# Optimization experiments

Measured on AMD Instinct MI355X. Metric: run time of the kernel, lower is better.

The kernel has to match this reference:

```python
import jax, jax.numpy as jnp
import numpy as np

BS, SEQ, DK = 4, 4096, 128

def setup_inputs() -> dict:
    key = jax.random.key(0)
    kq, kk, kv = jax.random.split(key, 3)
    q = jax.random.normal(kq, (BS, SEQ, DK), dtype=jnp.float32)
    k = jax.random.normal(kk, (BS, SEQ, DK), dtype=jnp.float32)
    v = jax.random.normal(kv, (BS, SEQ, DK), dtype=jnp.float32)
    return {"q": q, "k": k, "v": v}

def reference(q, k, v):
    d_k = q.shape[-1]
    # scores: [bs, s_q, s_k]
    scaled = jnp.einsum('bqd,bkd->bqk', q, k) / jnp.sqrt(jnp.asarray(d_k, q.dtype))
    # NOTE: original torch code applies softmax over dim=1 (query axis), faithfully reproduced here.
    attn = jax.nn.softmax(scaled, axis=1)
    return jnp.einsum('bqk,bkd->bqd', attn, v)
```

## Files before the change

### kernel.cpp

```cpp
#include <hip/hip_runtime.h>
#include <hip/hip_bf16.h>

#define BS  4
#define SEQ 4096
#define DK  128

#define C1_SCALE (1.4426950408889634f / 11.313708498984761f)

typedef __attribute__((ext_vector_type(8))) short bf16x8;
typedef __attribute__((ext_vector_type(4))) float f32x4;
typedef unsigned short ushort_t;

__device__ inline unsigned pk_bf16(float a, float b) {
    __hip_bfloat162 h = __float22bfloat162_rn(make_float2(a, b));
    union { __hip_bfloat162 h2; unsigned u; } cv;
    cv.h2 = h;
    return cv.u;
}

__device__ inline bf16x8 pk8(float4 a, float4 b) {
    union { bf16x8 v; unsigned u[4]; } r;
    r.u[0] = pk_bf16(a.x, a.y);
    r.u[1] = pk_bf16(a.z, a.w);
    r.u[2] = pk_bf16(b.x, b.y);
    r.u[3] = pk_bf16(b.z, b.w);
    return r.v;
}

__global__ __launch_bounds__(256) void cast_qk_sw(
    const float* __restrict__ Q, const float* __restrict__ K,
    ushort_t* __restrict__ Qb, ushort_t* __restrict__ Kb)
{
    const int g = blockIdx.x * 256 + threadIdx.x;
    const int q = g >> 4, ap = g & 15;
    const int a = ap ^ (q & 15);
    const float* src = Q + (size_t)q * DK + a * 8;
    float4 x = *(const float4*)src, y = *(const float4*)(src + 4);
    *(bf16x8*)(Qb + (size_t)g * 8) = pk8(x, y);
    src = K + (size_t)q * DK + a * 8;
    x = *(const float4*)src; y = *(const float4*)(src + 4);
    *(bf16x8*)(Kb + (size_t)g * 8) = pk8(x, y);
}

__global__ __launch_bounds__(256) void sdpa_lsum(
    const ushort_t* __restrict__ Qb, const ushort_t* __restrict__ Kb,
    float* __restrict__ lp)
{
    const int kt = blockIdx.x, qs = blockIdx.y, b = blockIdx.z;
    const int tid = threadIdx.x;
    const int w = tid >> 6, lane = tid & 63, ln = lane & 15, quad = lane >> 4;

    bf16x8 ka[2][4];
#pragma unroll
    for (int mt = 0; mt < 2; ++mt)
#pragma unroll
        for (int c = 0; c < 4; ++c)
            ka[mt][c] = *(const bf16x8*)(Kb +
                ((size_t)(b * SEQ) + kt * 128 + w * 32 + mt * 16 + ln) * DK +
                (((c * 4 + quad) ^ ln) * 8));

    float ls[2][4] = {};
    const ushort_t* qbase = Qb + ((size_t)(b * SEQ) + qs * 512 + ln) * DK;
    bf16x8 qf0[2][4], qf1[2][4];

#define L_PRE(QF, IT)                                                          \
    {                                                                          \
        _Pragma("unroll")                                                      \
        for (int nt = 0; nt < 2; ++nt)                                         \
            _Pragma("unroll")                                                  \
            for (int c = 0; c < 4; ++c)                                        \
                QF[nt][c] = *(const bf16x8*)(qbase +                           \
                    ((size_t)((IT) * 32 + nt * 16)) * DK +                     \
                    (((c * 4 + quad) ^ ln) * 8));                              \
    }
#define L_CMP(QF)                                                              \
    {                                                                          \
        _Pragma("unroll")                                                      \
        for (int mt = 0; mt < 2; ++mt)                                         \
            _Pragma("unroll")                                                  \
            for (int nt = 0; nt < 2; ++nt) {                                   \
                f32x4 s = {0.f, 0.f, 0.f, 0.f};                                \
                _Pragma("unroll")                                              \
                for (int c = 0; c < 4; ++c)                                    \
                    s = __builtin_amdgcn_mfma_f32_16x16x32_bf16(               \
                        ka[mt][c], QF[nt][c], s, 0, 0, 0);                     \
                _Pragma("unroll")                                              \
                for (int r = 0; r < 4; ++r)                                    \
                    ls[mt][r] += __builtin_amdgcn_exp2f(C1_SCALE * s[r]);      \
            }                                                                  \
    }
    L_PRE(qf0, 0)
    for (int ii = 0; ii < 8; ++ii) {
        const int i0 = 2 * ii;
        L_PRE(qf1, i0 + 1)
        L_CMP(qf0)
        if (ii < 7) L_PRE(qf0, i0 + 2)
        L_CMP(qf1)
    }
#undef L_PRE
#undef L_CMP

#pragma unroll
    for (int mt = 0; mt < 2; ++mt)
#pragma unroll
        for (int r = 0; r < 4; ++r) {
            float vv = ls[mt][r];
            vv += __shfl_xor(vv, 1);
            vv += __shfl_xor(vv, 2);
            vv += __shfl_xor(vv, 4);
            vv += __shfl_xor(vv, 8);
            ls[mt][r] = vv;
        }
    if (ln < 8) {
        int k = kt * 128 + w * 32 + (ln >> 2) * 16 + quad * 4 + (ln & 3);
        lp[((size_t)(qs * BS + b)) * SEQ + k] = ls[ln >> 2][ln & 3];
    }
}

__global__ __launch_bounds__(256) void vb_transpose(
    const float* __restrict__ V, const float* __restrict__ lp,
    ushort_t* __restrict__ VbT)
{
    __shared__ float Vl[64][132];
    __shared__ float Wl[64];

    const int kt = blockIdx.x, b = blockIdx.y;
    const int tid = threadIdx.x;
    const int k0 = kt * 64;
    {
        int r = tid >> 2, sg = tid & 3;
        const float* src = V + ((size_t)(b * SEQ) + k0 + r) * DK + sg * 32;
#pragma unroll
        for (int i = 0; i < 8; ++i)
            *(float4*)&Vl[r][sg * 32 + i * 4] = *(const float4*)(src + i * 4);
    }
    if (tid < 64) {
        float s = 0.f;
#pragma unroll
        for (int qs = 0; qs < 8; ++qs)
            s += lp[((size_t)(qs * BS + b)) * SEQ + k0 + tid];
        Wl[tid] = 1.0f / s;
    }
    __syncthreads();

    const int d = tid >> 1, kh = tid & 1;
    unsigned u[16];
#pragma unroll
    for (int j = 0; j < 16; ++j) {
        int row = kh * 32 + j * 2;
        u[j] = pk_bf16(Vl[row][d] * Wl[row], Vl[row + 1][d] * Wl[row + 1]);
    }
    ushort_t* dst = VbT + ((size_t)(b * DK) + d) * SEQ + k0 + kh * 32;
#pragma unroll
    for (int i = 0; i < 4; ++i) {
        uint4 t4; t4.x = u[i*4]; t4.y = u[i*4+1]; t4.z = u[i*4+2]; t4.w = u[i*4+3];
        *(uint4*)(dst + i * 8) = t4;
    }
}

__global__ __launch_bounds__(256) void sdpa_out(
    const ushort_t* __restrict__ Qb, const ushort_t* __restrict__ Kb,
    const ushort_t* __restrict__ VbT,
    float* __restrict__ Op, float* __restrict__ O, int use_partial)
{
    __shared__ ushort_t Pt[2][64 * 64];

    const int g  = blockIdx.x;
    const int qt = blockIdx.y;
    const int ks = g >> 2, b = g & 3;
    const int tid = threadIdx.x;
    const int w = tid >> 6, lane = tid & 63, ln = lane & 15, quad = lane >> 4;

    bf16x8 qa[4][4];
#pragma unroll
    for (int nt = 0; nt < 4; ++nt)
#pragma unroll
        for (int c = 0; c < 4; ++c)
            qa[c][nt] = *(const bf16x8*)(Qb +
                ((size_t)(b * SEQ) + qt * 64 + nt * 16 + ln) * DK +
                (((c * 4 + quad) ^ ln) * 8));

    f32x4 acc[4][2];
#pragma unroll
    for (int i = 0; i < 4; ++i)
#pragma unroll
        for (int j = 0; j < 2; ++j) acc[i][j] = (f32x4){0.f, 0.f, 0.f, 0.f};

    const ushort_t* kfp = Kb + ((size_t)(b * SEQ) + ks * 1024 + w * 16 + ln) * DK;
    const ushort_t* vfp = VbT + ((size_t)(b * DK) + w * 32 + ln) * SEQ + ks * 1024 + quad * 8;

    bf16x8 kf0[4], kf1[4], vf0[4], vf1[4];

#define QK_PHASE(P, KF)                                                        \
    {                                                                          \
        _Pragma("unroll")                                                      \
        for (int nt = 0; nt < 4; ++nt) {                                       \
            f32x4 s = {0.f, 0.f, 0.f, 0.f};                                    \
            _Pragma("unroll")                                                  \
            for (int c = 0; c < 4; ++c)                                        \
                s = __builtin_amdgcn_mfma_f32_16x16x32_bf16(KF[c], qa[c][nt], s, 0, 0, 0); \
            uint2 pw;                                                          \
            pw.x = pk_bf16(__builtin_amdgcn_exp2f(C1_SCALE * s[0]),            \
                           __builtin_amdgcn_exp2f(C1_SCALE * s[1]));           \
            pw.y = pk_bf16(__builtin_amdgcn_exp2f(C1_SCALE * s[2]),            \
                           __builtin_amdgcn_exp2f(C1_SCALE * s[3]));           \
            const int q = nt * 16 + ln;                                        \
            const int a16 = w * 2 + (quad >> 1);                               \
            *(uint2*)&Pt[P][q * 64 + ((a16 ^ (q & 7)) * 8) + (quad & 1) * 4] = pw; \
        }                                                                      \
    }
#define PREFETCH(KF, VF, I1)                                                   \
    {                                                                          \
        _Pragma("unroll")                                                      \
        for (int c = 0; c < 4; ++c)                                            \
            KF[c] = *(const bf16x8*)(kfp + (size_t)(I1) * 64 * DK +            \
                                     (((c * 4 + quad) ^ ln) * 8));             \
        _Pragma("unroll")                                                      \
        for (int dt = 0; dt < 2; ++dt)                                         \
            _Pragma("unroll")                                                  \
            for (int kc = 0; kc < 2; ++kc)                                     \
                VF[kc * 2 + dt] = *(const bf16x8*)(vfp +                       \
                    (size_t)dt * 16 * SEQ + (size_t)(I1) * 64 + kc * 32);      \
    }
#define PV_PHASE(P, VF)                                                        \
    {                                                                          \
        _Pragma("unroll")                                                      \
        for (int kc = 0; kc < 2; ++kc) {                                       \
            bf16x8 pa[4];                                                      \
            _Pragma("unroll")                                                  \
            for (int qf2 = 0; qf2 < 4; ++qf2)                                  \
                pa[qf2] = *(const bf16x8*)&Pt[P][(qf2 * 16 + ln) * 64 +        \
                                    (((kc * 4 + quad) ^ (ln & 7)) * 8)];       \
            _Pragma("unroll")                                                  \
            for (int qf2 = 0; qf2 < 4; ++qf2)                                  \
                _Pragma("unroll")                                              \
                for (int dt = 0; dt < 2; ++dt)                                 \
                    acc[qf2][dt] = __builtin_amdgcn_mfma_f32_16x16x32_bf16(    \
                        pa[qf2], VF[kc * 2 + dt], acc[qf2][dt], 0, 0, 0);      \
        }                                                                      \
    }

#pragma unroll
    for (int c = 0; c < 4; ++c)
        kf0[c] = *(const bf16x8*)(kfp + (((c * 4 + quad) ^ ln) * 8));
#pragma unroll
    for (int dt = 0; dt < 2; ++dt)
#pragma unroll
        for (int kc = 0; kc < 2; ++kc)
            vf0[kc * 2 + dt] = *(const bf16x8*)(vfp + (size_t)dt * 16 * SEQ + kc * 32);

    for (int ii = 0; ii < 8; ++ii) {
        const int i0 = 2 * ii;
        PREFETCH(kf1, vf1, i0 + 1)
        QK_PHASE(0, kf0)
        __syncthreads();
        PV_PHASE(0, vf0)
        if (ii < 7) PREFETCH(kf0, vf0, i0 + 2)
        QK_PHASE(1, kf1)
        __syncthreads();
        PV_PHASE(1, vf1)
    }
#undef QK_PHASE
#undef PREFETCH
#undef PV_PHASE

    if (use_partial) {
        float* dst = Op + (size_t)ks * ((size_t)BS * SEQ * DK) +
                     ((size_t)(b * SEQ) + qt * 64 + quad * 4) * DK + w * 32 + ln;
#pragma unroll
        for (int qf2 = 0; qf2 < 4; ++qf2)
#pragma unroll
            for (int dt = 0; dt < 2; ++dt)
#pragma unroll
                for (int r = 0; r < 4; ++r)
                    dst[((size_t)(qf2 * 16 + r)) * DK + dt * 16] = acc[qf2][dt][r];
    } else {
#pragma unroll
        for (int qf2 = 0; qf2 < 4; ++qf2)
#pragma unroll
            for (int dt = 0; dt < 2; ++dt)
#pragma unroll
                for (int r = 0; r < 4; ++r)
                    atomicAdd(&O[((size_t)(b * SEQ) + qt * 64 + qf2 * 16 + quad * 4 + r) * DK +
                                 w * 32 + dt * 16 + ln], acc[qf2][dt][r]);
    }
}

__global__ __launch_bounds__(256) void reduce4(
    const float* __restrict__ Op, float* __restrict__ O)
{
    const size_t N = (size_t)BS * SEQ * DK;
    size_t i = ((size_t)blockIdx.x * 256 + threadIdx.x) * 4;
    float4 a0 = *(const float4*)(Op + i);
    float4 a1 = *(const float4*)(Op + N + i);
    float4 a2 = *(const float4*)(Op + 2 * N + i);
    float4 a3 = *(const float4*)(Op + 3 * N + i);
    float4 r;
    r.x = a0.x + a1.x + a2.x + a3.x;
    r.y = a0.y + a1.y + a2.y + a3.y;
    r.z = a0.z + a1.z + a2.z + a3.z;
    r.w = a0.w + a1.w + a2.w + a3.w;
    *(float4*)(O + i) = r;
}

extern "C" void kernel_launch(void* const* d_in, const int* in_sizes, int n_in,
                              void* d_out, int out_size, void* d_ws, size_t ws_size,
                              hipStream_t stream) {
    const float* q = (const float*)d_in[0];
    const float* k = (const float*)d_in[1];
    const float* v = (const float*)d_in[2];
    float* out = (float*)d_out;

    const size_t QKV = (size_t)BS * SEQ * DK;
    float*    lp  = (float*)d_ws;
    ushort_t* Qb  = (ushort_t*)((char*)d_ws + (1 << 20));
    ushort_t* Kb  = Qb + QKV;
    ushort_t* VbT = Kb + QKV;
    float*    Op  = (float*)(VbT + QKV);

    const size_t need_p = (1u << 20) + 3 * QKV * 2 + 4 * QKV * sizeof(float);

    cast_qk_sw<<<dim3(BS * SEQ * 16 / 256), 256, 0, stream>>>(q, k, Qb, Kb);
    sdpa_lsum  <<<dim3(32, 8, 4), 256, 0, stream>>>(Qb, Kb, lp);
    vb_transpose<<<dim3(64, 4),   256, 0, stream>>>(v, lp, VbT);

    if (ws_size >= need_p) {
        sdpa_out<<<dim3(16, 64), 256, 0, stream>>>(Qb, Kb, VbT, Op, out, 1);
        reduce4 <<<dim3(BS * SEQ * DK / 4 / 256), 256, 0, stream>>>(Op, out);
    } else {
        hipMemsetAsync(out, 0, QKV * sizeof(float), stream);
        sdpa_out<<<dim3(16, 64), 256, 0, stream>>>(Qb, Kb, VbT, nullptr, out, 0);
    }
}
```

Baseline: 183.7 us.

## Give each wave its own query rows in sdpa_out, dropping block barriers

The output kernel is restructured so each wave owns 16 query rows and the full 128-wide head dimension. Each wave writes its probabilities to a private LDS slice, which removes the block-wide __syncthreads between the QK and PV phases. Every wave now loads all K and V tiles, so global and L2 traffic per block goes up. The softmax scale is folded into Q during the bf16 cast, and s_setprio is wrapped around the MFMA chains in both kernels. launch_bounds now asks for two blocks per CU.

```diff
diff --git a/kernel.cpp b/kernel.cpp
--- a/kernel.cpp
+++ b/kernel.cpp
@@ -36,10 +36,12 @@
     const int a = ap ^ (q & 15);
     const float* src = Q + (size_t)q * DK + a * 8;
     float4 x = *(const float4*)src, y = *(const float4*)(src + 4);
+    x.x *= C1_SCALE; x.y *= C1_SCALE; x.z *= C1_SCALE; x.w *= C1_SCALE;
+    y.x *= C1_SCALE; y.y *= C1_SCALE; y.z *= C1_SCALE; y.w *= C1_SCALE;
     *(bf16x8*)(Qb + (size_t)g * 8) = pk8(x, y);
     src = K + (size_t)q * DK + a * 8;
-    x = *(const float4*)src; y = *(const float4*)(src + 4);
-    *(bf16x8*)(Kb + (size_t)g * 8) = pk8(x, y);
+    float4 x2 = *(const float4*)src, y2 = *(const float4*)(src + 4);
+    *(bf16x8*)(Kb + (size_t)g * 8) = pk8(x2, y2);
 }
 
 __global__ __launch_bounds__(256) void sdpa_lsum(
@@ -80,13 +82,15 @@
             _Pragma("unroll")                                                  \
             for (int nt = 0; nt < 2; ++nt) {                                   \
                 f32x4 s = {0.f, 0.f, 0.f, 0.f};                                \
+                __builtin_amdgcn_s_setprio(1);                                 \
                 _Pragma("unroll")                                              \
                 for (int c = 0; c < 4; ++c)                                    \
                     s = __builtin_amdgcn_mfma_f32_16x16x32_bf16(               \
                         ka[mt][c], QF[nt][c], s, 0, 0, 0);                     \
+                __builtin_amdgcn_s_setprio(0);                                 \
                 _Pragma("unroll")                                              \
                 for (int r = 0; r < 4; ++r)                                    \
-                    ls[mt][r] += __builtin_amdgcn_exp2f(C1_SCALE * s[r]);      \
+                    ls[mt][r] += __builtin_amdgcn_exp2f(s[r]);                 \
             }                                                                  \
     }
     L_PRE(qf0, 0)
@@ -158,12 +162,12 @@
     }
 }
 
-__global__ __launch_bounds__(256) void sdpa_out(
+__global__ __launch_bounds__(256, 2) void sdpa_out(
     const ushort_t* __restrict__ Qb, const ushort_t* __restrict__ Kb,
     const ushort_t* __restrict__ VbT,
     float* __restrict__ Op, float* __restrict__ O, int use_partial)
 {
-    __shared__ ushort_t Pt[2][64 * 64];
+    __shared__ ushort_t Pt[4][1024];
 
     const int g  = blockIdx.x;
     const int qt = blockIdx.y;
@@ -171,118 +175,93 @@
     const int tid = threadIdx.x;
     const int w = tid >> 6, lane = tid & 63, ln = lane & 15, quad = lane >> 4;
 
-    bf16x8 qa[4][4];
-#pragma unroll
-    for (int nt = 0; nt < 4; ++nt)
-#pragma unroll
-        for (int c = 0; c < 4; ++c)
-            qa[c][nt] = *(const bf16x8*)(Qb +
-                ((size_t)(b * SEQ) + qt * 64 + nt * 16 + ln) * DK +
-                (((c * 4 + quad) ^ ln) * 8));
-
-    f32x4 acc[4][2];
-#pragma unroll
-    for (int i = 0; i < 4; ++i)
-#pragma unroll
-        for (int j = 0; j < 2; ++j) acc[i][j] = (f32x4){0.f, 0.f, 0.f, 0.f};
-
-    const ushort_t* kfp = Kb + ((size_t)(b * SEQ) + ks * 1024 + w * 16 + ln) * DK;
-    const ushort_t* vfp = VbT + ((size_t)(b * DK) + w * 32 + ln) * SEQ + ks * 1024 + quad * 8;
-
-    bf16x8 kf0[4], kf1[4], vf0[4], vf1[4];
-
-#define QK_PHASE(P, KF)                                                        \
-    {                                                                          \
-        _Pragma("unroll")                                                      \
-        for (int nt = 0; nt < 4; ++nt) {                                       \
-            f32x4 s = {0.f, 0.f, 0.f, 0.f};                                    \
+    bf16x8 qa[4];
+#pragma unroll
+    for (int c = 0; c < 4; ++c)
+        qa[c] = *(const bf16x8*)(Qb +
+            ((size_t)(b * SEQ) + qt * 64 + w * 16 + ln) * DK +
+            (((c * 4 + quad) ^ ln) * 8));
+
+    f32x4 acc[8];
+#pragma unroll
+    for (int i = 0; i < 8; ++i) acc[i] = (f32x4){0.f, 0.f, 0.f, 0.f};
+
+    const ushort_t* kfp = Kb + ((size_t)(b * SEQ) + ks * 1024 + ln) * DK;
+    const ushort_t* vfp = VbT + ((size_t)(b * DK) + ln) * SEQ + ks * 1024 + quad * 8;
+
+    bf16x8 ka[2][4], vf[8];
+
+#define LOADK(NIT, NH)                                                         \
+    {                                                                          \
+        _Pragma("unroll")                                                      \
+        for (int kt2 = 0; kt2 < 2; ++kt2)                                      \
             _Pragma("unroll")                                                  \
             for (int c = 0; c < 4; ++c)                                        \
-                s = __builtin_amdgcn_mfma_f32_16x16x32_bf16(KF[c], qa[c][nt], s, 0, 0, 0); \
-            uint2 pw;                                                          \
-            pw.x = pk_bf16(__builtin_amdgcn_exp2f(C1_SCALE * s[0]),            \
-                           __builtin_amdgcn_exp2f(C1_SCALE * s[1]));           \
-            pw.y = pk_bf16(__builtin_amdgcn_exp2f(C1_SCALE * s[2]),            \
-                           __builtin_amdgcn_exp2f(C1_SCALE * s[3]));           \
-            const int q = nt * 16 + ln;                                        \
-            const int a16 = w * 2 + (quad >> 1);                               \
-            *(uint2*)&Pt[P][q * 64 + ((a16 ^ (q & 7)) * 8) + (quad & 1) * 4] = pw; \
-        }                                                                      \
-    }
-#define PREFETCH(KF, VF, I1)                                                   \
-    {                                                                          \
+                ka[kt2][c] = *(const bf16x8*)(kfp +                            \
+                    (size_t)((NIT) * 64 + (NH) * 32 + kt2 * 16) * DK +         \
+                    (((c * 4 + quad) ^ ln) * 8));                              \
+    }
+#define LOADV(NIT, NH)                                                         \
+    {                                                                          \
+        _Pragma("unroll")                                                      \
+        for (int dt = 0; dt < 8; ++dt)                                         \
+            vf[dt] = *(const bf16x8*)(vfp + (size_t)dt * 16 * SEQ +            \
+                                      (NIT) * 64 + (NH) * 32);                 \
+    }
+#define HALF(H, NIT, NH)                                                       \
+    {                                                                          \
+        f32x4 s0 = {0.f, 0.f, 0.f, 0.f}, s1 = {0.f, 0.f, 0.f, 0.f};           \
+        __builtin_amdgcn_s_setprio(1);                                         \
         _Pragma("unroll")                                                      \
         for (int c = 0; c < 4; ++c)                                            \
-            KF[c] = *(const bf16x8*)(kfp + (size_t)(I1) * 64 * DK +            \
-                                     (((c * 4 + quad) ^ ln) * 8));             \
-        _Pragma("unroll")                                                      \
-        for (int dt = 0; dt < 2; ++dt)                                         \
-            _Pragma("unroll")                                                  \
-            for (int kc = 0; kc < 2; ++kc)                                     \
-                VF[kc * 2 + dt] = *(const bf16x8*)(vfp +                       \
-                    (size_t)dt * 16 * SEQ + (size_t)(I1) * 64 + kc * 32);      \
-    }
-#define PV_PHASE(P, VF)                                                        \
-    {                                                                          \
-        _Pragma("unroll")                                                      \
-        for (int kc = 0; kc < 2; ++kc) {                                       \
-            bf16x8 pa[4];                                                      \
-            _Pragma("unroll")                                                  \
-            for (int qf2 = 0; qf2 < 4; ++qf2)                                  \
-                pa[qf2] = *(const bf16x8*)&Pt[P][(qf2 * 16 + ln) * 64 +        \
-                                    (((kc * 4 + quad) ^ (ln & 7)) * 8)];       \
-            _Pragma("unroll")                                                  \
-            for (int qf2 = 0; qf2 < 4; ++qf2)                                  \
-                _Pragma("unroll")                                              \
-                for (int dt = 0; dt < 2; ++dt)                                 \
-                    acc[qf2][dt] = __builtin_amdgcn_mfma_f32_16x16x32_bf16(    \
-                        pa[qf2], VF[kc * 2 + dt], acc[qf2][dt], 0, 0, 0);      \
-        }                                                                      \
-    }
-
-#pragma unroll
-    for (int c = 0; c < 4; ++c)
-        kf0[c] = *(const bf16x8*)(kfp + (((c * 4 + quad) ^ ln) * 8));
-#pragma unroll
-    for (int dt = 0; dt < 2; ++dt)
-#pragma unroll
-        for (int kc = 0; kc < 2; ++kc)
-            vf0[kc * 2 + dt] = *(const bf16x8*)(vfp + (size_t)dt * 16 * SEQ + kc * 32);
-
-    for (int ii = 0; ii < 8; ++ii) {
-        const int i0 = 2 * ii;
-        PREFETCH(kf1, vf1, i0 + 1)
-        QK_PHASE(0, kf0)
-        __syncthreads();
-        PV_PHASE(0, vf0)
-        if (ii < 7) PREFETCH(kf0, vf0, i0 + 2)
-        QK_PHASE(1, kf1)
-        __syncthreads();
-        PV_PHASE(1, vf1)
-    }
-#undef QK_PHASE
-#undef PREFETCH
-#undef PV_PHASE
+            s0 = __builtin_amdgcn_mfma_f32_16x16x32_bf16(ka[0][c], qa[c], s0, 0, 0, 0); \
+        _Pragma("unroll")                                                      \
+        for (int c = 0; c < 4; ++c)                                            \
+            s1 = __builtin_amdgcn_mfma_f32_16x16x32_bf16(ka[1][c], qa[c], s1, 0, 0, 0); \
+        __builtin_amdgcn_s_setprio(0);                                         \
+        LOADK(NIT, NH)                                                         \
+        uint2 p0, p1;                                                          \
+        p0.x = pk_bf16(__builtin_amdgcn_exp2f(s0[0]), __builtin_amdgcn_exp2f(s0[1])); \
+        p0.y = pk_bf16(__builtin_amdgcn_exp2f(s0[2]), __builtin_amdgcn_exp2f(s0[3])); \
+        p1.x = pk_bf16(__builtin_amdgcn_exp2f(s1[0]), __builtin_amdgcn_exp2f(s1[1])); \
+        p1.y = pk_bf16(__builtin_amdgcn_exp2f(s1[2]), __builtin_amdgcn_exp2f(s1[3])); \
+        *(uint2*)&Pt[w][ln * 64 + ((((H) * 4 + 0 + (quad >> 1)) ^ (ln & 7)) * 8) + (quad & 1) * 4] = p0; \
+        *(uint2*)&Pt[w][ln * 64 + ((((H) * 4 + 2 + (quad >> 1)) ^ (ln & 7)) * 8) + (quad & 1) * 4] = p1; \
+        bf16x8 pa = *(const bf16x8*)&Pt[w][ln * 64 + ((((H) * 4 + quad) ^ (ln & 7)) * 8)]; \
+        __builtin_amdgcn_s_setprio(1);                                         \
+        _Pragma("unroll")                                                      \
+        for (int dt = 0; dt < 8; ++dt)                                         \
+            acc[dt] = __builtin_amdgcn_mfma_f32_16x16x32_bf16(pa, vf[dt], acc[dt], 0, 0, 0); \
+        __builtin_amdgcn_s_setprio(0);                                         \
+        LOADV(NIT, NH)                                                         \
+    }
+
+    LOADK(0, 0)
+    LOADV(0, 0)
+    for (int it = 0; it < 16; ++it) {
+        HALF(0, it, 1)
+        const int nx = (it < 15) ? it + 1 : 15;
+        HALF(1, nx, 0)
+    }
+#undef LOADK
+#undef LOADV
+#undef HALF
 
     if (use_partial) {
         float* dst = Op + (size_t)ks * ((size_t)BS * SEQ * DK) +
-                     ((size_t)(b * SEQ) + qt * 64 + quad * 4) * DK + w * 32 + ln;
-#pragma unroll
-        for (int qf2 = 0; qf2 < 4; ++qf2)
-#pragma unroll
-            for (int dt = 0; dt < 2; ++dt)
-#pragma unroll
-                for (int r = 0; r < 4; ++r)
-                    dst[((size_t)(qf2 * 16 + r)) * DK + dt * 16] = acc[qf2][dt][r];
+                     ((size_t)(b * SEQ) + qt * 64 + w * 16 + quad * 4) * DK + ln;
+#pragma unroll
+        for (int dt = 0; dt < 8; ++dt)
+#pragma unroll
+            for (int r = 0; r < 4; ++r)
+                dst[(size_t)r * DK + dt * 16] = acc[dt][r];
     } else {
 #pragma unroll
-        for (int qf2 = 0; qf2 < 4; ++qf2)
-#pragma unroll
-            for (int dt = 0; dt < 2; ++dt)
-#pragma unroll
-                for (int r = 0; r < 4; ++r)
-                    atomicAdd(&O[((size_t)(b * SEQ) + qt * 64 + qf2 * 16 + quad * 4 + r) * DK +
-                                 w * 32 + dt * 16 + ln], acc[qf2][dt][r]);
+        for (int dt = 0; dt < 8; ++dt)
+#pragma unroll
+            for (int r = 0; r < 4; ++r)
+                atomicAdd(&O[((size_t)(b * SEQ) + qt * 64 + w * 16 + quad * 4 + r) * DK +
+                             dt * 16 + ln], acc[dt][r]);
     }
 }
 
```

Result: slower. 266.5 us (+45.0%).

## Stage Q/K/V tiles through LDS with async global_load_lds and fold softmax scale

Applied to the files above, without the earlier changes.

Both attention kernels now copy Q (row-sum kernel) and K/V (output kernel) tiles into double-buffered shared memory with `global_load_lds` DMA, then read MFMA operands from LDS. Before, each wave loaded its fragments straight from global memory into registers. The softmax scale is folded into Q during the bf16 cast, which removes one multiply per score before each exp2. MFMA blocks are wrapped in `s_setprio` raises. The intent is fewer redundant global loads and lower register pressure, at the cost of more LDS use (lower occupancy), an extra barrier per phase, and a single shared P buffer.

```diff
diff --git a/kernel.cpp b/kernel.cpp
--- a/kernel.cpp
+++ b/kernel.cpp
@@ -27,6 +27,13 @@
     return r.v;
 }
 
+__device__ inline void gld_lds16(const ushort_t* g, ushort_t* l) {
+    __builtin_amdgcn_global_load_lds(
+        (const __attribute__((address_space(1))) unsigned int*)g,
+        (__attribute__((address_space(3))) unsigned int*)l,
+        16, 0, 0);
+}
+
 __global__ __launch_bounds__(256) void cast_qk_sw(
     const float* __restrict__ Q, const float* __restrict__ K,
     ushort_t* __restrict__ Qb, ushort_t* __restrict__ Kb)
@@ -36,16 +43,20 @@
     const int a = ap ^ (q & 15);
     const float* src = Q + (size_t)q * DK + a * 8;
     float4 x = *(const float4*)src, y = *(const float4*)(src + 4);
+    x.x *= C1_SCALE; x.y *= C1_SCALE; x.z *= C1_SCALE; x.w *= C1_SCALE;
+    y.x *= C1_SCALE; y.y *= C1_SCALE; y.z *= C1_SCALE; y.w *= C1_SCALE;
     *(bf16x8*)(Qb + (size_t)g * 8) = pk8(x, y);
     src = K + (size_t)q * DK + a * 8;
-    x = *(const float4*)src; y = *(const float4*)(src + 4);
-    *(bf16x8*)(Kb + (size_t)g * 8) = pk8(x, y);
+    float4 x2 = *(const float4*)src, y2 = *(const float4*)(src + 4);
+    *(bf16x8*)(Kb + (size_t)g * 8) = pk8(x2, y2);
 }
 
 __global__ __launch_bounds__(256) void sdpa_lsum(
     const ushort_t* __restrict__ Qb, const ushort_t* __restrict__ Kb,
     float* __restrict__ lp)
 {
+    __shared__ ushort_t Qs[2][4096];
+
     const int kt = blockIdx.x, qs = blockIdx.y, b = blockIdx.z;
     const int tid = threadIdx.x;
     const int w = tid >> 6, lane = tid & 63, ln = lane & 15, quad = lane >> 4;
@@ -60,45 +71,54 @@
                 (((c * 4 + quad) ^ ln) * 8));
 
     float ls[2][4] = {};
-    const ushort_t* qbase = Qb + ((size_t)(b * SEQ) + qs * 512 + ln) * DK;
-    bf16x8 qf0[2][4], qf1[2][4];
-
-#define L_PRE(QF, IT)                                                          \
-    {                                                                          \
+    const ushort_t* qtb = Qb + ((size_t)(b * SEQ + qs * 512)) * DK;
+
+#define A_DMA(BUF, I)                                                          \
+    {                                                                          \
+        _Pragma("unroll")                                                      \
+        for (int j = 0; j < 2; ++j)                                            \
+            gld_lds16(qtb + (size_t)(I) * 4096 + (j * 256 + tid) * 8,          \
+                      &Qs[BUF][(j * 256 + w * 64) * 8]);                       \
+    }
+
+#define A_CMP(BUF)                                                             \
+    {                                                                          \
+        bf16x8 qf[2][4];                                                       \
         _Pragma("unroll")                                                      \
         for (int nt = 0; nt < 2; ++nt)                                         \
             _Pragma("unroll")                                                  \
             for (int c = 0; c < 4; ++c)                                        \
-                QF[nt][c] = *(const bf16x8*)(qbase +                           \
-                    ((size_t)((IT) * 32 + nt * 16)) * DK +                     \
-                    (((c * 4 + quad) ^ ln) * 8));                              \
-    }
-#define L_CMP(QF)                                                              \
-    {                                                                          \
+                qf[nt][c] = *(const bf16x8*)&Qs[BUF][(nt * 16 + ln) * 128 +    \
+                                    (((c * 4 + quad) ^ ln) * 8)];              \
         _Pragma("unroll")                                                      \
         for (int mt = 0; mt < 2; ++mt)                                         \
             _Pragma("unroll")                                                  \
             for (int nt = 0; nt < 2; ++nt) {                                   \
                 f32x4 s = {0.f, 0.f, 0.f, 0.f};                                \
+                __builtin_amdgcn_s_setprio(1);                                 \
                 _Pragma("unroll")                                              \
                 for (int c = 0; c < 4; ++c)                                    \
                     s = __builtin_amdgcn_mfma_f32_16x16x32_bf16(               \
-                        ka[mt][c], QF[nt][c], s, 0, 0, 0);                     \
+                        ka[mt][c], qf[nt][c], s, 0, 0, 0);                     \
+                __builtin_amdgcn_s_setprio(0);                                 \
                 _Pragma("unroll")                                              \
                 for (int r = 0; r < 4; ++r)                                    \
-                    ls[mt][r] += __builtin_amdgcn_exp2f(C1_SCALE * s[r]);      \
+                    ls[mt][r] += __builtin_amdgcn_exp2f(s[r]);                 \
             }                                                                  \
     }
-    L_PRE(qf0, 0)
+
+    A_DMA(0, 0)
     for (int ii = 0; ii < 8; ++ii) {
         const int i0 = 2 * ii;
-        L_PRE(qf1, i0 + 1)
-        L_CMP(qf0)
-        if (ii < 7) L_PRE(qf0, i0 + 2)
-        L_CMP(qf1)
-    }
-#undef L_PRE
-#undef L_CMP
+        __syncthreads();
+        A_DMA(1, i0 + 1)
+        A_CMP(0)
+        __syncthreads();
+        if (ii < 7) A_DMA(0, i0 + 2)
+        A_CMP(1)
+    }
+#undef A_DMA
+#undef A_CMP
 
 #pragma unroll
     for (int mt = 0; mt < 2; ++mt)
@@ -163,7 +183,9 @@
     const ushort_t* __restrict__ VbT,
     float* __restrict__ Op, float* __restrict__ O, int use_partial)
 {
-    __shared__ ushort_t Pt[2][64 * 64];
+    __shared__ ushort_t Kt[2][8192];
+    __shared__ ushort_t Vt[2][8192];
+    __shared__ ushort_t Pt[4096];
 
     const int g  = blockIdx.x;
     const int qt = blockIdx.y;
@@ -186,82 +208,84 @@
 #pragma unroll
         for (int j = 0; j < 2; ++j) acc[i][j] = (f32x4){0.f, 0.f, 0.f, 0.f};
 
-    const ushort_t* kfp = Kb + ((size_t)(b * SEQ) + ks * 1024 + w * 16 + ln) * DK;
-    const ushort_t* vfp = VbT + ((size_t)(b * DK) + w * 32 + ln) * SEQ + ks * 1024 + quad * 8;
-
-    bf16x8 kf0[4], kf1[4], vf0[4], vf1[4];
-
-#define QK_PHASE(P, KF)                                                        \
-    {                                                                          \
+    const ushort_t* ksrc = Kb + ((size_t)(b * SEQ) + ks * 1024) * DK;
+    const ushort_t* vsrc = VbT + ((size_t)(b * DK)) * SEQ + ks * 1024;
+    const int vd = tid >> 3, vap = tid & 7;
+
+#define O_DMA(BUF, PH)                                                         \
+    {                                                                          \
+        _Pragma("unroll")                                                      \
+        for (int j = 0; j < 4; ++j)                                            \
+            gld_lds16(ksrc + (size_t)(PH) * 64 * DK + (j * 256 + tid) * 8,     \
+                      &Kt[BUF][(j * 256 + w * 64) * 8]);                       \
+        _Pragma("unroll")                                                      \
+        for (int j = 0; j < 4; ++j)                                            \
+            gld_lds16(vsrc + (size_t)(j * 32 + vd) * SEQ + (PH) * 64 +         \
+                          ((vap ^ (vd & 7)) * 8),                              \
+                      &Vt[BUF][(j * 256 + w * 64) * 8]);                       \
+    }
+
+#define QK_PHASE(BUF)                                                          \
+    {                                                                          \
+        bf16x8 kf[4];                                                          \
+        _Pragma("unroll")                                                      \
+        for (int c = 0; c < 4; ++c)                                            \
+            kf[c] = *(const bf16x8*)&Kt[BUF][(w * 16 + ln) * 128 +             \
+                                             (((c * 4 + quad) ^ ln) * 8)];     \
         _Pragma("unroll")                                                      \
         for (int nt = 0; nt < 4; ++nt) {                                       \
             f32x4 s = {0.f, 0.f, 0.f, 0.f};                                    \
+            __builtin_amdgcn_s_setprio(1);                                     \
             _Pragma("unroll")                                                  \
             for (int c = 0; c < 4; ++c)                                        \
-                s = __builtin_amdgcn_mfma_f32_16x16x32_bf16(KF[c], qa[c][nt], s, 0, 0, 0); \
+                s = __builtin_amdgcn_mfma_f32_16x16x32_bf16(kf[c], qa[c][nt], s, 0, 0, 0); \
+            __builtin_amdgcn_s_setprio(0);                                     \
             uint2 pw;                                                          \
-            pw.x = pk_bf16(__builtin_amdgcn_exp2f(C1_SCALE * s[0]),            \
-                           __builtin_amdgcn_exp2f(C1_SCALE * s[1]));           \
-            pw.y = pk_bf16(__builtin_amdgcn_exp2f(C1_SCALE * s[2]),            \
-                           __builtin_amdgcn_exp2f(C1_SCALE * s[3]));           \
+            pw.x = pk_bf16(__builtin_amdgcn_exp2f(s[0]),                       \
+                           __builtin_amdgcn_exp2f(s[1]));                      \
+            pw.y = pk_bf16(__builtin_amdgcn_exp2f(s[2]),                       \
+                           __builtin_amdgcn_exp2f(s[3]));                      \
             const int q = nt * 16 + ln;                                        \
             const int a16 = w * 2 + (quad >> 1);                               \
-            *(uint2*)&Pt[P][q * 64 + ((a16 ^ (q & 7)) * 8) + (quad & 1) * 4] = pw; \
+            *(uint2*)&Pt[q * 64 + ((a16 ^ (q & 7)) * 8) + (quad & 1) * 4] = pw; \
         }                                                                      \
     }
-#define PREFETCH(KF, VF, I1)                                                   \
-    {                                                                          \
-        _Pragma("unroll")                                                      \
-        for (int c = 0; c < 4; ++c)                                            \
-            KF[c] = *(const bf16x8*)(kfp + (size_t)(I1) * 64 * DK +            \
-                                     (((c * 4 + quad) ^ ln) * 8));             \
-        _Pragma("unroll")                                                      \
-        for (int dt = 0; dt < 2; ++dt)                                         \
-            _Pragma("unroll")                                                  \
-            for (int kc = 0; kc < 2; ++kc)                                     \
-                VF[kc * 2 + dt] = *(const bf16x8*)(vfp +                       \
-                    (size_t)dt * 16 * SEQ + (size_t)(I1) * 64 + kc * 32);      \
-    }
-#define PV_PHASE(P, VF)                                                        \
+
+#define PV_PHASE(BUF)                                                          \
     {                                                                          \
         _Pragma("unroll")                                                      \
         for (int kc = 0; kc < 2; ++kc) {                                       \
-            bf16x8 pa[4];                                                      \
+            bf16x8 pa[4], vfr[2];                                              \
             _Pragma("unroll")                                                  \
             for (int qf2 = 0; qf2 < 4; ++qf2)                                  \
-                pa[qf2] = *(const bf16x8*)&Pt[P][(qf2 * 16 + ln) * 64 +        \
+                pa[qf2] = *(const bf16x8*)&Pt[(qf2 * 16 + ln) * 64 +           \
                                     (((kc * 4 + quad) ^ (ln & 7)) * 8)];       \
+            _Pragma("unroll")                                                  \
+            for (int dt = 0; dt < 2; ++dt)                                     \
+                vfr[dt] = *(const bf16x8*)&Vt[BUF][(w * 32 + dt * 16 + ln) * 64 + \
+                                    (((kc * 4 + quad) ^ (ln & 7)) * 8)];       \
+            __builtin_amdgcn_s_setprio(1);                                     \
             _Pragma("unroll")                                                  \
             for (int qf2 = 0; qf2 < 4; ++qf2)                                  \
                 _Pragma("unroll")                                              \
                 for (int dt = 0; dt < 2; ++dt)                                 \
                     acc[qf2][dt] = __builtin_amdgcn_mfma_f32_16x16x32_bf16(    \
-                        pa[qf2], VF[kc * 2 + dt], acc[qf2][dt], 0, 0, 0);      \
+                        pa[qf2], vfr[dt], acc[qf2][dt], 0, 0, 0);              \
+            __builtin_amdgcn_s_setprio(0);                                     \
         }                                                                      \
     }
 
-#pragma unroll
-    for (int c = 0; c < 4; ++c)
-        kf0[c] = *(const bf16x8*)(kfp + (((c * 4 + quad) ^ ln) * 8));
-#pragma unroll
-    for (int dt = 0; dt < 2; ++dt)
-#pragma unroll
-        for (int kc = 0; kc < 2; ++kc)
-            vf0[kc * 2 + dt] = *(const bf16x8*)(vfp + (size_t)dt * 16 * SEQ + kc * 32);
-
-    for (int ii = 0; ii < 8; ++ii) {
-        const int i0 = 2 * ii;
-        PREFETCH(kf1, vf1, i0 + 1)
-        QK_PHASE(0, kf0)
+    O_DMA(0, 0)
+    for (int ph = 0; ph < 16; ++ph) {
+        const int cur = ph & 1;
         __syncthreads();
-        PV_PHASE(0, vf0)
-        if (ii < 7) PREFETCH(kf0, vf0, i0 + 2)
-        QK_PHASE(1, kf1)
+        if (ph < 15) O_DMA(cur ^ 1, ph + 1)
+        QK_PHASE(cur)
         __syncthreads();
-        PV_PHASE(1, vf1)
-    }
+        PV_PHASE(cur)
+    }
+#undef O_DMA
 #undef QK_PHASE
-#undef PREFETCH
 #undef PV_PHASE
 
     if (use_partial) {
```

After: 172.4 us. 1.07x faster.
